# Optimization experiments

Measured on AMD Instinct MI355X. Metric: run time of the kernel, lower is better.

Reference implementation:

```python
import jax, jax.numpy as jnp
import numpy as np

NUM_ELEM = 62
DEGREE = 3
M = 64  # matrix_size = sqrt(layer_sizes[0]) = sqrt(4096)
IN_DIM, H = 4096, 2048
N_POINTS = 2_097_152


def _glorot(k, shape):
    lim = np.float32(np.sqrt(2.0 / (shape[0] + shape[1])))
    return jax.random.normal(k, shape, jnp.float32) * lim


def setup_inputs() -> dict:
    key = jax.random.key(0)
    ks = jax.random.split(key, 4)
    points = jax.random.uniform(ks[0], (N_POINTS, 2), jnp.float32)
    # first coordinate lives in [-1, 1) (original maps it via (x+1)/2)
    points = points.at[:, 0].set(points[:, 0] * 2.0 - 1.0)
    return {
        "points": points,
        "W1": _glorot(ks[1], (IN_DIM, H)), "b1": jnp.zeros((H,), jnp.float32),
        "W2": _glorot(ks[2], (H, H)),      "b2": jnp.zeros((H,), jnp.float32),
        "W3": _glorot(ks[3], (H, 1)),      "b3": jnp.zeros((1,), jnp.float32),
    }


def _quadratic(t):
    # tfg bspline._quadratic: 3 quadratic B-spline basis functions of t in [0,1)
    return jnp.stack([(1.0 - t) ** 2 * 0.5, -t * t + t + 0.5, t * t * 0.5], axis=-1)


def _spline(coord):
    p = coord * NUM_ELEM
    pos = jnp.minimum(jnp.floor(p).astype(jnp.int32) + 1, NUM_ELEM)  # tf.cond clamp
    return _quadratic(jnp.mod(p, 1.0)), pos


def reference(points, W1, b1, W2, b2, W3, b3):
    # cofs = eye(4096); identity @ W1 == W1, so the first Dense reduces to W1 + b1
    h = jnp.tanh(W1 + b1)
    h = jnp.tanh(h @ W2 + b2)
    out = jnp.tanh(h @ W3 + b3)          # [4096, 1]
    u = out.reshape(M, M) * 3.0           # control-point grid [64, 64]

    x = (points[:, 0] + 1.0) * 0.5
    y = points[:, 1]
    bx, px = _spline(x)                   # bx: [N,3], px: [N]
    by, py = _spline(y)
    offs = jnp.arange(DEGREE)
    ix = px[:, None] - 1 + offs           # [N,3] row indices into u
    iy = py[:, None] - 1 + offs           # [N,3] col indices into u
    Wn = u[ix[:, :, None], iy[:, None, :]]  # [N,3,3] local control-point windows
    # sum_{i,j} W[i,j] * splines_x[i] * splines_y[j]  (meshgrid orientation)
    return jnp.einsum('nij,ni,nj->n', Wn, bx, by)
```

## Files before the change

### kernel.cpp

```cpp
#include <hip/hip_runtime.h>
#include <stdint.h>

#define IN_DIM 4096
#define H_DIM  2048
#define NPTS   2097152

typedef short  bf16x8  __attribute__((ext_vector_type(8)));
typedef float  floatx4 __attribute__((ext_vector_type(4)));

#define AS1 __attribute__((address_space(1)))
#define AS3 __attribute__((address_space(3)))

__device__ __forceinline__ unsigned short f2bf(float f) {
    unsigned u = __float_as_uint(f);
    unsigned r = (u + 0x7FFFu + ((u >> 16) & 1u)) >> 16;
    return (unsigned short)r;
}

__device__ __forceinline__ float tanh_fast(float x) {
    float e = __builtin_amdgcn_exp2f(x * 2.885390081777927f);
    return 1.0f - 2.0f * __builtin_amdgcn_rcpf(e + 1.0f);
}

__global__ void prep_all(const float* __restrict__ W1, const float* __restrict__ b1,
                         const float* __restrict__ W2,
                         unsigned short* __restrict__ hbf, unsigned short* __restrict__ W2T,
                         float* __restrict__ rowsum) {
    __shared__ unsigned short tile[64][66];
    int b = blockIdx.x;
    if (b < 8192) {
        if (b < 16) rowsum[b * 256 + threadIdx.x] = 0.0f;
        int idx = (b * 256 + threadIdx.x) * 4;
        float4 w = *(const float4*)(W1 + idx);
        float4 bb = *(const float4*)(b1 + (idx & (H_DIM - 1)));
        ushort4 o;
        o.x = f2bf(tanh_fast(w.x + bb.x));
        o.y = f2bf(tanh_fast(w.y + bb.y));
        o.z = f2bf(tanh_fast(w.z + bb.z));
        o.w = f2bf(tanh_fast(w.w + bb.w));
        *(ushort4*)(hbf + idx) = o;
    } else {
        int bb = b - 8192;
        int k0 = (bb >> 5) * 64, n0 = (bb & 31) * 64;
        for (int idx = threadIdx.x; idx < 64 * 64; idx += 256) {
            int r = idx >> 6, c = idx & 63;
            tile[c][r] = f2bf(W2[(size_t)(k0 + r) * H_DIM + n0 + c]);
        }
        __syncthreads();
        for (int idx = threadIdx.x; idx < 64 * 64; idx += 256) {
            int r = idx >> 6, c = idx & 63;
            W2T[(size_t)(n0 + r) * H_DIM + k0 + c] = tile[r][c];
        }
    }
}

#define BK 64
__global__ __launch_bounds__(256, 4) void gemm_fused(
    const unsigned short* __restrict__ A,
    const unsigned short* __restrict__ BT,
    const float* __restrict__ b2, const float* __restrict__ W3,
    float* __restrict__ rowsum) {
    __shared__ __align__(16) unsigned short As[128 * BK];
    __shared__ __align__(16) unsigned short Bs[64 * BK];
    const int K = H_DIM;
    const int t = threadIdx.x;
    const int w = t >> 6, l = t & 63;
    const int lane16 = l & 15, quad = l >> 4;
    const int wr = w >> 1, wc = w & 1;

    const int bid = blockIdx.x;
    const int xcd = bid & 7, idx = bid >> 3;
    const int by = (xcd >> 1) * 8 + (idx >> 4);
    const int bx = (xcd & 1) * 16 + (idx & 15);
    const int rowBase = by * 128;
    const int colBase = bx * 64;

    const int sRow = l >> 3;
    const int sChunk = (l & 7) ^ sRow;
    const size_t laneOff = (size_t)sRow * K + sChunk * 8;

    const unsigned short* aBase = A  + (size_t)(rowBase + w * 32) * K + laneOff;
    const unsigned short* bBase = BT + (size_t)(colBase + w * 16) * K + laneOff;

    floatx4 acc[4][2];
    floatx4 zero = {0.f, 0.f, 0.f, 0.f};
#pragma unroll
    for (int i = 0; i < 4; ++i)
#pragma unroll
        for (int j = 0; j < 2; ++j) acc[i][j] = zero;

    for (int k0 = 0; k0 < K; k0 += BK) {
        __syncthreads();
#pragma unroll
        for (int i = 0; i < 4; ++i)
            __builtin_amdgcn_global_load_lds(
                (const AS1 void*)(aBase + (size_t)i * 8 * K + k0),
                (AS3 void*)(As + (w * 32 + i * 8) * 64), 16, 0, 0);
#pragma unroll
        for (int i = 0; i < 2; ++i)
            __builtin_amdgcn_global_load_lds(
                (const AS1 void*)(bBase + (size_t)i * 8 * K + k0),
                (AS3 void*)(Bs + (w * 16 + i * 8) * 64), 16, 0, 0);
        __syncthreads();

#pragma unroll
        for (int s = 0; s < 2; ++s) {
            const int cs = (s * 4 + quad) ^ (lane16 & 7);
            bf16x8 af[4], bfr[2];
#pragma unroll
            for (int mi = 0; mi < 4; ++mi)
                af[mi] = *(const bf16x8*)(As + (wr * 64 + mi * 16 + lane16) * 64 + cs * 8);
#pragma unroll
            for (int ni = 0; ni < 2; ++ni)
                bfr[ni] = *(const bf16x8*)(Bs + (wc * 32 + ni * 16 + lane16) * 64 + cs * 8);
#pragma unroll
            for (int mi = 0; mi < 4; ++mi)
#pragma unroll
                for (int ni = 0; ni < 2; ++ni)
                    acc[mi][ni] = __builtin_amdgcn_mfma_f32_16x16x32_bf16(
                        af[mi], bfr[ni], acc[mi][ni], 0, 0, 0);
        }
    }

    const int rowG = rowBase + wr * 64;
#pragma unroll
    for (int mi = 0; mi < 4; ++mi) {
#pragma unroll
        for (int r = 0; r < 4; ++r) {
            float s = 0.f;
#pragma unroll
            for (int ni = 0; ni < 2; ++ni) {
                int col = colBase + wc * 32 + ni * 16 + lane16;
                float v = acc[mi][ni][r] + b2[col];
                s += tanh_fast(v) * W3[col];
            }
#pragma unroll
            for (int off = 1; off < 16; off <<= 1) s += __shfl_xor(s, off, 64);
            if (lane16 == 0)
                atomicAdd(&rowsum[rowG + mi * 16 + quad * 4 + r], s);
        }
    }
}

__device__ __forceinline__ float spline_eval(const float* us, float ptx, float pty) {
    float x = (ptx + 1.0f) * 0.5f;
    float px = x * 62.0f, py = pty * 62.0f;
    float fx = floorf(px), fy = floorf(py);
    int posx = min((int)fx + 1, 62);
    int posy = min((int)fy + 1, 62);
    float tx = px - fx, ty = py - fy;
    float bx0 = 0.5f * (1.f - tx) * (1.f - tx);
    float bx1 = -tx * tx + tx + 0.5f;
    float bx2 = 0.5f * tx * tx;
    float by0 = 0.5f * (1.f - ty) * (1.f - ty);
    float by1 = -ty * ty + ty + 0.5f;
    float by2 = 0.5f * ty * ty;
    const float* r0 = &us[(posx - 1) * 64 + (posy - 1)];
    const float* r1 = r0 + 64;
    const float* r2 = r1 + 64;
    float s0 = r0[0] * by0 + r0[1] * by1 + r0[2] * by2;
    float s1 = r1[0] * by0 + r1[1] * by1 + r1[2] * by2;
    float s2 = r2[0] * by0 + r2[1] * by1 + r2[2] * by2;
    return bx0 * s0 + bx1 * s1 + bx2 * s2;
}

__global__ void spline_kernel(const float4* __restrict__ pts,
                              const float* __restrict__ rowsum,
                              const float* __restrict__ b3,
                              float2* __restrict__ out, int npairs) {
    __shared__ float us[4096];
    float bias = b3[0];
    for (int i = threadIdx.x; i < 4096; i += blockDim.x)
        us[i] = 3.0f * tanh_fast(rowsum[i] + bias);
    __syncthreads();
    int stride = gridDim.x * blockDim.x;
    for (int idx = blockIdx.x * blockDim.x + threadIdx.x; idx < npairs; idx += stride) {
        float4 p2 = pts[idx];
        float2 o;
        o.x = spline_eval(us, p2.x, p2.y);
        o.y = spline_eval(us, p2.z, p2.w);
        out[idx] = o;
    }
}

extern "C" void kernel_launch(void* const* d_in, const int* in_sizes, int n_in,
                              void* d_out, int out_size, void* d_ws, size_t ws_size,
                              hipStream_t stream) {
    const float* points = (const float*)d_in[0];
    const float* W1 = (const float*)d_in[1];
    const float* b1 = (const float*)d_in[2];
    const float* W2 = (const float*)d_in[3];
    const float* b2 = (const float*)d_in[4];
    const float* W3 = (const float*)d_in[5];
    const float* b3 = (const float*)d_in[6];
    float* out = (float*)d_out;

    char* ws = (char*)d_ws;
    unsigned short* hbf = (unsigned short*)ws;
    unsigned short* w2t = (unsigned short*)(ws + 16777216);
    float* rowsum = (float*)(ws + 25165824);

    prep_all<<<8192 + 1024, 256, 0, stream>>>(W1, b1, W2, hbf, w2t, rowsum);
    gemm_fused<<<1024, 256, 0, stream>>>(hbf, w2t, b2, W3, rowsum);
    spline_kernel<<<1024, 256, 0, stream>>>((const float4*)points, rowsum, b3,
                                            (float2*)out, NPTS / 2);
}
```

Before: 169.4 us.

## Load GEMM B operand directly into registers with double-buffered prefetch

The B tile (transposed W2) no longer goes through shared memory. Each lane now loads its bf16x8 MFMA fragments straight from global memory into registers. Two register buffers alternate so the next K-step's B loads overlap the current step's MFMAs. Barriers become explicit waitcnt plus s_barrier. This removes the B LDS traffic and halves the LDS footprint, but waves that share a column range now fetch the same B data redundantly, and the loads stride across rows instead of being contiguous, which may hurt global/L2 efficiency.

```diff
diff --git a/kernel.cpp b/kernel.cpp
--- a/kernel.cpp
+++ b/kernel.cpp
@@ -61,7 +61,6 @@
     const float* __restrict__ b2, const float* __restrict__ W3,
     float* __restrict__ rowsum) {
     __shared__ __align__(16) unsigned short As[128 * BK];
-    __shared__ __align__(16) unsigned short Bs[64 * BK];
     const int K = H_DIM;
     const int t = threadIdx.x;
     const int w = t >> 6, l = t & 63;
@@ -78,9 +77,10 @@
     const int sRow = l >> 3;
     const int sChunk = (l & 7) ^ sRow;
     const size_t laneOff = (size_t)sRow * K + sChunk * 8;
-
-    const unsigned short* aBase = A  + (size_t)(rowBase + w * 32) * K + laneOff;
-    const unsigned short* bBase = BT + (size_t)(colBase + w * 16) * K + laneOff;
+    const unsigned short* aBase = A + (size_t)(rowBase + w * 32) * K + laneOff;
+
+    const unsigned short* bDir =
+        BT + (size_t)(colBase + wc * 32 + lane16) * K + quad * 8;
 
     floatx4 acc[4][2];
     floatx4 zero = {0.f, 0.f, 0.f, 0.f};
@@ -89,38 +89,71 @@
 #pragma unroll
         for (int j = 0; j < 2; ++j) acc[i][j] = zero;
 
-    for (int k0 = 0; k0 < K; k0 += BK) {
-        __syncthreads();
-#pragma unroll
-        for (int i = 0; i < 4; ++i)
-            __builtin_amdgcn_global_load_lds(
-                (const AS1 void*)(aBase + (size_t)i * 8 * K + k0),
-                (AS3 void*)(As + (w * 32 + i * 8) * 64), 16, 0, 0);
-#pragma unroll
-        for (int i = 0; i < 2; ++i)
-            __builtin_amdgcn_global_load_lds(
-                (const AS1 void*)(bBase + (size_t)i * 8 * K + k0),
-                (AS3 void*)(Bs + (w * 16 + i * 8) * 64), 16, 0, 0);
-        __syncthreads();
-
-#pragma unroll
-        for (int s = 0; s < 2; ++s) {
-            const int cs = (s * 4 + quad) ^ (lane16 & 7);
-            bf16x8 af[4], bfr[2];
-#pragma unroll
-            for (int mi = 0; mi < 4; ++mi)
-                af[mi] = *(const bf16x8*)(As + (wr * 64 + mi * 16 + lane16) * 64 + cs * 8);
-#pragma unroll
-            for (int ni = 0; ni < 2; ++ni)
-                bfr[ni] = *(const bf16x8*)(Bs + (wc * 32 + ni * 16 + lane16) * 64 + cs * 8);
-#pragma unroll
-            for (int mi = 0; mi < 4; ++mi)
-#pragma unroll
-                for (int ni = 0; ni < 2; ++ni)
-                    acc[mi][ni] = __builtin_amdgcn_mfma_f32_16x16x32_bf16(
-                        af[mi], bfr[ni], acc[mi][ni], 0, 0, 0);
-        }
-    }
+    bf16x8 bA[2][2], bB[2][2];
+
+#define STAGEA(k0)                                                             \
+    {                                                                          \
+        _Pragma("unroll")                                                      \
+        for (int i = 0; i < 4; ++i)                                            \
+            __builtin_amdgcn_global_load_lds(                                  \
+                (const AS1 void*)(aBase + (size_t)i * 8 * K + (k0)),           \
+                (AS3 void*)(As + (w * 32 + i * 8) * 64), 16, 0, 0);            \
+    }
+
+#define LOADB(dst, k0)                                                         \
+    {                                                                          \
+        dst[0][0] = *(const bf16x8*)(bDir + (k0));                             \
+        dst[0][1] = *(const bf16x8*)(bDir + (size_t)16 * K + (k0));            \
+        dst[1][0] = *(const bf16x8*)(bDir + (k0) + 32);                        \
+        dst[1][1] = *(const bf16x8*)(bDir + (size_t)16 * K + (k0) + 32);       \
+    }
+
+#define COMPUTE(breg)                                                          \
+    {                                                                          \
+        _Pragma("unroll")                                                      \
+        for (int s = 0; s < 2; ++s) {                                          \
+            const int cs = (s * 4 + quad) ^ (lane16 & 7);                      \
+            bf16x8 af[4];                                                      \
+            _Pragma("unroll")                                                  \
+            for (int mi = 0; mi < 4; ++mi)                                     \
+                af[mi] = *(const bf16x8*)(As + (wr * 64 + mi * 16 + lane16) * 64 + cs * 8); \
+            _Pragma("unroll")                                                  \
+            for (int mi = 0; mi < 4; ++mi)                                     \
+                _Pragma("unroll")                                              \
+                for (int ni = 0; ni < 2; ++ni)                                 \
+                    acc[mi][ni] = __builtin_amdgcn_mfma_f32_16x16x32_bf16(     \
+                        af[mi], breg[s][ni], acc[mi][ni], 0, 0, 0);            \
+        }                                                                      \
+    }
+
+#define TOPSYNC()                                                              \
+    asm volatile("s_waitcnt lgkmcnt(0)" ::: "memory");                         \
+    __builtin_amdgcn_s_barrier();
+
+#define VMSYNC()                                                               \
+    asm volatile("s_waitcnt vmcnt(0)" ::: "memory");                           \
+    __builtin_amdgcn_s_barrier();
+
+    LOADB(bA, 0);
+
+    for (int k0 = 0; k0 < K; k0 += 2 * BK) {
+        TOPSYNC();
+        STAGEA(k0);
+        VMSYNC();
+        LOADB(bB, k0 + BK);
+        COMPUTE(bA);
+        TOPSYNC();
+        STAGEA(k0 + BK);
+        VMSYNC();
+        LOADB(bA, (k0 + 2 * BK) & (K - 1));
+        COMPUTE(bB);
+    }
+
+#undef STAGEA
+#undef LOADB
+#undef COMPUTE
+#undef TOPSYNC
+#undef VMSYNC
 
     const int rowG = rowBase + wr * 64;
 #pragma unroll
```

Result: slower. 207.0 us (+22.2%).
